# Optimization experiments

Hardware: AMD Instinct MI355X
Metric: run time of the kernel (lower is better)

Reference implementation:

```python
import jax, jax.numpy as jnp
import numpy as np

B, T, C, H = 4, 2048, 1024, 16
D = C // H  # head dim = 64

def setup_inputs() -> dict:
    key = jax.random.key(0)
    k1, k2, k3 = jax.random.split(key, 3)
    y = jax.random.normal(k1, (B, T, C), dtype=jnp.float32)
    W_attn = jax.random.normal(k2, (C, 3 * C), dtype=jnp.float32) * (1.0 / np.sqrt(C))
    b_attn = jnp.zeros((3 * C,), dtype=jnp.float32)
    W_proj = jax.random.normal(k3, (C, C), dtype=jnp.float32) * (1.0 / np.sqrt(C))
    b_proj = jnp.zeros((C,), dtype=jnp.float32)
    return {"y": y, "W_attn": W_attn, "b_attn": b_attn, "W_proj": W_proj, "b_proj": b_proj}

def reference(y, W_attn, b_attn, W_proj, b_proj):
    # qkv projection: [B,T,C] @ [C,3C] -> split into q,k,v
    qkv = y @ W_attn + b_attn
    q, k, v = jnp.split(qkv, 3, axis=-1)
    # [B,T,C] -> [B,H,T,D]
    q = q.reshape(B, T, H, D).swapaxes(1, 2)
    k = k.reshape(B, T, H, D).swapaxes(1, 2)
    v = v.reshape(B, T, H, D).swapaxes(1, 2)
    # scaled dot-product attention, non-causal (config default), dropout=0
    att = jnp.einsum('bhtd,bhrd->bhtr', q, k) * (1.0 / jnp.sqrt(jnp.float32(D)))
    att = jax.nn.softmax(att, axis=-1)
    out = jnp.einsum('bhts,bhsd->bhtd', att, v)
    out = out.swapaxes(1, 2).reshape(B, T, C)
    return out @ W_proj + b_proj
```

## Files before the change

kernel.cpp:

```cpp
#include <hip/hip_runtime.h>
#include <hip/hip_bf16.h>
#include <stdint.h>

#define B_ 4
#define T_ 2048
#define C_ 1024
#define H_ 16
#define D_ 64

typedef short bf16x8 __attribute__((ext_vector_type(8)));
typedef float f32x4 __attribute__((ext_vector_type(4)));
typedef unsigned short u16;

#define QSCALE 0.18033688011112042f

__device__ __forceinline__ u16 f2bf(float f) {
    __hip_bfloat16 h = __float2bfloat16(f);
    return *reinterpret_cast<u16*>(&h);
}

__device__ __forceinline__ float fexp2(float x) {
    float r;
    asm("v_exp_f32 %0, %1" : "=v"(r) : "v"(x));
    return r;
}

__device__ __forceinline__ void gload16(const void* g, void* l) {
    __builtin_amdgcn_global_load_lds(
        (const __attribute__((address_space(1))) unsigned int*)g,
        (__attribute__((address_space(3))) unsigned int*)l, 16, 0, 0);
}

__global__ void k_prep(const float* __restrict__ y, u16* __restrict__ y_bf,
                       const float* __restrict__ Wa, u16* __restrict__ WaT,
                       const float* __restrict__ Wp, u16* __restrict__ WpT) {
    const int bid = blockIdx.x, tid = threadIdx.x;
    if (bid < 8192) {
        int i = (bid * 256 + tid) * 4;
        float4 f = *reinterpret_cast<const float4*>(y + i);
        ushort4 o;
        o.x = f2bf(f.x); o.y = f2bf(f.y); o.z = f2bf(f.z); o.w = f2bf(f.w);
        *reinterpret_cast<ushort4*>(y_bf + i) = o;
        return;
    }
    __shared__ float tile[32][33];
    const float* src; u16* dst; int R, Cc, bx, by;
    if (bid < 8192 + 3072) {
        int idx = bid - 8192;
        src = Wa; dst = WaT; R = 1024; Cc = 3072;
        bx = idx % 96; by = idx / 96;
    } else {
        int idx = bid - 11264;
        src = Wp; dst = WpT; R = 1024; Cc = 1024;
        bx = idx & 31; by = idx >> 5;
    }
    int c0 = bx * 32, r0 = by * 32;
    int tx = tid & 31, ty = tid >> 5;
#pragma unroll
    for (int i = 0; i < 4; i++)
        tile[ty + i * 8][tx] = src[(size_t)(r0 + ty + i * 8) * Cc + c0 + tx];
    __syncthreads();
#pragma unroll
    for (int i = 0; i < 4; i++)
        dst[(size_t)(c0 + ty + i * 8) * R + r0 + tx] = f2bf(tile[tx][ty + i * 8]);
}

template <int EPI>
__launch_bounds__(256, 2)
__global__ void k_gemm(const u16* __restrict__ A, const u16* __restrict__ Bt,
                       const float* __restrict__ bias, int K, int N,
                       float* __restrict__ outf,
                       u16* __restrict__ qw, u16* __restrict__ kw, u16* __restrict__ vw) {
    __shared__ u16 As[128 * 64];
    __shared__ u16 Bs[128 * 64];
    const int tid = threadIdx.x;
    const int lane = tid & 63, w = tid >> 6;
    const int m0 = blockIdx.x * 128, n0 = blockIdx.y * 128;
    const int wm = (w >> 1) * 64, wn = (w & 1) * 64;
    const int lr = lane & 15, lg = lane >> 4;

    f32x4 acc[4][4];
#pragma unroll
    for (int i = 0; i < 4; i++)
#pragma unroll
        for (int j = 0; j < 4; j++) acc[i][j] = (f32x4){0.f, 0.f, 0.f, 0.f};

    const int nk = K >> 6;
    for (int kt = 0; kt < nk; ++kt) {
        const int k0 = kt * 64;
#pragma unroll
        for (int i = 0; i < 4; i++) {
            int c = i * 256 + tid;
            int row = c >> 3, k8 = (c & 7) << 3;
            gload16(A + (size_t)(m0 + row) * K + k0 + k8, (char*)As + i * 4096 + w * 1024);
            gload16(Bt + (size_t)(n0 + row) * K + k0 + k8, (char*)Bs + i * 4096 + w * 1024);
        }
        __syncthreads();
#pragma unroll
        for (int kk = 0; kk < 2; ++kk) {
            bf16x8 af[4], bfr[4];
#pragma unroll
            for (int mf = 0; mf < 4; ++mf)
                af[mf] = *reinterpret_cast<const bf16x8*>(&As[(wm + mf * 16 + lr) * 64 + kk * 32 + lg * 8]);
#pragma unroll
            for (int nf = 0; nf < 4; ++nf)
                bfr[nf] = *reinterpret_cast<const bf16x8*>(&Bs[(wn + nf * 16 + lr) * 64 + kk * 32 + lg * 8]);
#pragma unroll
            for (int mf = 0; mf < 4; ++mf)
#pragma unroll
                for (int nf = 0; nf < 4; ++nf)
                    acc[mf][nf] = __builtin_amdgcn_mfma_f32_16x16x32_bf16(af[mf], bfr[nf], acc[mf][nf], 0, 0, 0);
        }
        __syncthreads();
    }

    if (EPI == 0) {
#pragma unroll
        for (int mf = 0; mf < 4; ++mf)
#pragma unroll
            for (int nf = 0; nf < 4; ++nf) {
                int ng = n0 + wn + nf * 16 + lr;
                float bs = bias[ng];
#pragma unroll
                for (int r = 0; r < 4; ++r) {
                    int mg = m0 + wm + mf * 16 + lg * 4 + r;
                    outf[(size_t)mg * N + ng] = acc[mf][nf][r] + bs;
                }
            }
    } else {
        const int sec = n0 >> 10;
        const float sc = (sec == 0) ? QSCALE : 1.0f;
#pragma unroll
        for (int mf = 0; mf < 4; ++mf)
#pragma unroll
            for (int nf = 0; nf < 4; ++nf) {
                int ng = n0 + wn + nf * 16 + lr;
                float bs = bias[ng];
                int hd = ng & 1023;
                int h = hd >> 6, d = hd & 63;
                int mgb = m0 + wm + mf * 16 + lg * 4;
                int b = mgb >> 11, t0v = mgb & 2047;
                if (sec == 2) {
                    ushort4 pk;
                    pk.x = f2bf(acc[mf][nf][0] + bs);
                    pk.y = f2bf(acc[mf][nf][1] + bs);
                    pk.z = f2bf(acc[mf][nf][2] + bs);
                    pk.w = f2bf(acc[mf][nf][3] + bs);
                    *reinterpret_cast<ushort4*>(&vw[((size_t)(b * H_ + h) * D_ + d) * T_ + t0v]) = pk;
                } else {
                    u16* dst = (sec == 0) ? qw : kw;
#pragma unroll
                    for (int r = 0; r < 4; ++r)
                        dst[((size_t)(b * H_ + h) * T_ + t0v + r) * D_ + d] = f2bf((acc[mf][nf][r] + bs) * sc);
                }
            }
    }
}

__launch_bounds__(256, 4)
__global__ void k_attn(const u16* __restrict__ qw, const u16* __restrict__ kw,
                       const u16* __restrict__ vw, u16* __restrict__ attn) {
    __shared__ u16 Ks[2][64][64];
    __shared__ u16 Vs[2][64][64];
    const int tid = threadIdx.x, lane = tid & 63, w = tid >> 6;
    const int lr = lane & 15, lg = lane >> 4;
    const int bid = blockIdx.x;
    const int logical = (bid & 7) * 128 + (bid >> 3);
    const int bh = logical >> 4, qb = logical & 15;
    const int b = bh >> 4, h = bh & 15;
    const int q0 = qb * 128 + w * 32;
    const u16* qbase = qw + (size_t)bh * T_ * D_;
    const u16* kbase = kw + (size_t)bh * T_ * D_;
    const u16* vbase = vw + (size_t)bh * D_ * T_;

    bf16x8 qf[2][2];
#pragma unroll
    for (int jq = 0; jq < 2; jq++)
#pragma unroll
        for (int kd = 0; kd < 2; kd++)
            qf[jq][kd] = *reinterpret_cast<const bf16x8*>(
                &qbase[(size_t)(q0 + jq * 16 + lr) * D_ + kd * 32 + lg * 8]);

    auto stageK = [&](int kt, int buf) {
#pragma unroll
        for (int i = 0; i < 2; i++) {
            int idx = i * 256 + tid;
            int row = idx >> 3, ch = idx & 7;
            int gch = ch ^ ((row & 3) | (((row >> 3) & 1) << 2));
            gload16(kbase + ((size_t)(kt * 64 + row) * 64 + gch * 8),
                    (char*)&Ks[buf][0][0] + i * 4096 + w * 1024);
        }
    };
    auto stageV = [&](int kt, int buf) {
#pragma unroll
        for (int i = 0; i < 2; i++) {
            int idx = i * 256 + tid;
            int row = idx >> 3, ch = idx & 7;
            int gch = ch ^ (row & 7);
            gload16(vbase + ((size_t)row * T_ + kt * 64 + gch * 8),
                    (char*)&Vs[buf][0][0] + i * 4096 + w * 1024);
        }
    };

    f32x4 o[4][2];
#pragma unroll
    for (int md = 0; md < 4; md++)
#pragma unroll
        for (int jq = 0; jq < 2; jq++) o[md][jq] = (f32x4){0.f, 0.f, 0.f, 0.f};
    float l_run[2] = {0.f, 0.f};

    const int karow_base = ((lr >> 2) << 3) + (lr & 3);
    const int skl = ((lr & 3) | (((lr >> 2) & 1) << 2)) << 4;

    const int NT = T_ / 64;
    stageK(0, 0);
    stageV(0, 0);

    for (int kt = 0; kt < NT; ++kt) {
        const int cur = kt & 1;
        if (kt + 1 < NT) {
            stageK(kt + 1, cur ^ 1);
            stageV(kt + 1, cur ^ 1);
            asm volatile("s_waitcnt vmcnt(4)" ::: "memory");
        } else {
            asm volatile("s_waitcnt vmcnt(0)" ::: "memory");
        }
        __builtin_amdgcn_s_barrier();

        bf16x8 pfrag[2][2];
#pragma unroll
        for (int g = 0; g < 2; g++) {
            f32x4 st[2][2];
#pragma unroll
            for (int t = 0; t < 2; t++)
#pragma unroll
                for (int jq = 0; jq < 2; jq++) st[t][jq] = (f32x4){0.f, 0.f, 0.f, 0.f};
            __builtin_amdgcn_s_setprio(1);
#pragma unroll
            for (int t = 0; t < 2; t++) {
                int row = g * 32 + karow_base + t * 4;
#pragma unroll
                for (int kd = 0; kd < 2; kd++) {
                    bf16x8 ka = *reinterpret_cast<const bf16x8*>(
                        (const char*)&Ks[cur][0][0] + row * 128 + ((kd * 64 + lg * 16) ^ skl));
#pragma unroll
                    for (int jq = 0; jq < 2; jq++)
                        st[t][jq] = __builtin_amdgcn_mfma_f32_16x16x32_bf16(ka, qf[jq][kd], st[t][jq], 0, 0, 0);
                }
            }
            __builtin_amdgcn_s_setprio(0);
#pragma unroll
            for (int jq = 0; jq < 2; jq++) {
                float p0 = fexp2(st[0][jq][0]), p1 = fexp2(st[0][jq][1]);
                float p2 = fexp2(st[0][jq][2]), p3 = fexp2(st[0][jq][3]);
                float p4 = fexp2(st[1][jq][0]), p5 = fexp2(st[1][jq][1]);
                float p6 = fexp2(st[1][jq][2]), p7 = fexp2(st[1][jq][3]);
                l_run[jq] += ((p0 + p1) + (p2 + p3)) + ((p4 + p5) + (p6 + p7));
                pfrag[jq][g] = (bf16x8){(short)f2bf(p0), (short)f2bf(p1),
                                        (short)f2bf(p2), (short)f2bf(p3),
                                        (short)f2bf(p4), (short)f2bf(p5),
                                        (short)f2bf(p6), (short)f2bf(p7)};
            }
        }

#pragma unroll
        for (int g = 0; g < 2; g++) {
            bf16x8 va[4];
#pragma unroll
            for (int md = 0; md < 4; md++) {
                int row = md * 16 + lr;
                va[md] = *reinterpret_cast<const bf16x8*>(
                    (const char*)&Vs[cur][0][0] + row * 128 + ((g * 64 + lg * 16) ^ ((row & 7) << 4)));
            }
            __builtin_amdgcn_s_setprio(1);
#pragma unroll
            for (int md = 0; md < 4; md++)
#pragma unroll
                for (int jq = 0; jq < 2; jq++)
                    o[md][jq] = __builtin_amdgcn_mfma_f32_16x16x32_bf16(va[md], pfrag[jq][g], o[md][jq], 0, 0, 0);
            __builtin_amdgcn_s_setprio(0);
        }

        __builtin_amdgcn_s_barrier();
    }

#pragma unroll
    for (int jq = 0; jq < 2; jq++) {
        float l = l_run[jq];
        l += __shfl_xor(l, 16);
        l += __shfl_xor(l, 32);
        float rinv = 1.f / l;
        int q = q0 + jq * 16 + lr;
#pragma unroll
        for (int md = 0; md < 4; md++) {
            int d0 = md * 16 + lg * 4;
            ushort4 pk;
            pk.x = f2bf(o[md][jq][0] * rinv);
            pk.y = f2bf(o[md][jq][1] * rinv);
            pk.z = f2bf(o[md][jq][2] * rinv);
            pk.w = f2bf(o[md][jq][3] * rinv);
            *reinterpret_cast<ushort4*>(&attn[((size_t)(b * T_ + q)) * C_ + h * D_ + d0]) = pk;
        }
    }
}

extern "C" void kernel_launch(void* const* d_in, const int* in_sizes, int n_in,
                              void* d_out, int out_size, void* d_ws, size_t ws_size,
                              hipStream_t stream) {
    const float* y = (const float*)d_in[0];
    const float* W_attn = (const float*)d_in[1];
    const float* b_attn = (const float*)d_in[2];
    const float* W_proj = (const float*)d_in[3];
    const float* b_proj = (const float*)d_in[4];

    char* ws = (char*)d_ws;
    u16* y_bf = (u16*)(ws);
    u16* WaT  = (u16*)(ws + 16777216);
    u16* WpT  = (u16*)(ws + 16777216 + 6291456);
    u16* q_ws = (u16*)(ws + 25165824);
    u16* k_ws = (u16*)(ws + 25165824 + 16777216);
    u16* v_ws = (u16*)(ws + 25165824 + 33554432);
    u16* attn = (u16*)(ws + 25165824 + 50331648);

    k_prep<<<12288, 256, 0, stream>>>(y, y_bf, W_attn, WaT, W_proj, WpT);
    k_gemm<1><<<dim3(64, 24), 256, 0, stream>>>(y_bf, WaT, b_attn, 1024, 3072,
                                                nullptr, q_ws, k_ws, v_ws);
    k_attn<<<1024, 256, 0, stream>>>(q_ws, k_ws, v_ws, attn);
    k_gemm<0><<<dim3(64, 8), 256, 0, stream>>>(attn, WpT, b_proj, 1024, 1024,
                                               (float*)d_out, nullptr, nullptr, nullptr);
}
```

Measured before the change: 195.8 us.

## Software-pipeline attention loop: overlap PV of previous tile with QK/exp of current

Restructures the attention inner loop so the P·V MFMAs for tile k-1 are issued in the same phase as the QK^T MFMAs and exp for tile k. Two P-fragment register sets alternate, and the loop is unrolled by two. V gets a third LDS buffer so the previous V tile stays live while the next one is being loaded. The aim is to hide exp/convert latency behind matrix ops and give the scheduler more independent MFMA work, at the cost of extra registers and LDS that could reduce occupancy.

```diff
diff --git a/kernel.cpp b/kernel.cpp
--- a/kernel.cpp
+++ b/kernel.cpp
@@ -157,11 +157,75 @@
     }
 }
 
+#define ATTN_STAGE_K(kt, buf) do {                                            \
+    _Pragma("unroll") for (int i_ = 0; i_ < 2; i_++) {                        \
+        int idx_ = i_ * 256 + tid;                                            \
+        int row_ = idx_ >> 3, ch_ = idx_ & 7;                                 \
+        int gch_ = ch_ ^ ((row_ & 3) | (((row_ >> 3) & 1) << 2));             \
+        gload16(kbase + ((size_t)((kt) * 64 + row_) * 64 + gch_ * 8),         \
+                (char*)&Ks[0][0][0] + (buf) * 8192 + i_ * 4096 + w * 1024);   \
+    } } while (0)
+
+#define ATTN_STAGE_V(kt, buf) do {                                            \
+    _Pragma("unroll") for (int i_ = 0; i_ < 2; i_++) {                        \
+        int idx_ = i_ * 256 + tid;                                            \
+        int row_ = idx_ >> 3, ch_ = idx_ & 7;                                 \
+        int gch_ = ch_ ^ (row_ & 7);                                          \
+        gload16(vbase + ((size_t)row_ * T_ + (kt) * 64 + gch_ * 8),           \
+                (char*)&Vs[0][0][0] + (buf) * 8192 + i_ * 4096 + w * 1024);   \
+    } } while (0)
+
+#define ATTN_PV(PF) do {                                                      \
+    const char* Vp_ = (const char*)&Vs[0][0][0] + vprv * 8192;                \
+    __builtin_amdgcn_s_setprio(1);                                            \
+    _Pragma("unroll") for (int g_ = 0; g_ < 2; g_++) {                        \
+        _Pragma("unroll") for (int md_ = 0; md_ < 4; md_++) {                 \
+            int row_ = md_ * 16 + lr;                                         \
+            bf16x8 va_ = *reinterpret_cast<const bf16x8*>(                    \
+                Vp_ + row_ * 128 + ((g_ * 64 + lg * 16) ^ ((row_ & 7) << 4)));\
+            _Pragma("unroll") for (int jq_ = 0; jq_ < 2; jq_++)               \
+                o[md_][jq_] = __builtin_amdgcn_mfma_f32_16x16x32_bf16(        \
+                    va_, PF[jq_][g_], o[md_][jq_], 0, 0, 0);                  \
+        } }                                                                   \
+    __builtin_amdgcn_s_setprio(0); } while (0)
+
+#define ATTN_QKEXP(PF) do {                                                   \
+    const char* Kc_ = (const char*)&Ks[0][0][0] + kcur * 8192;                \
+    _Pragma("unroll") for (int g_ = 0; g_ < 2; g_++) {                        \
+        f32x4 st_[2][2];                                                      \
+        _Pragma("unroll") for (int t_ = 0; t_ < 2; t_++)                      \
+            _Pragma("unroll") for (int jq_ = 0; jq_ < 2; jq_++)               \
+                st_[t_][jq_] = (f32x4){0.f, 0.f, 0.f, 0.f};                   \
+        __builtin_amdgcn_s_setprio(1);                                        \
+        _Pragma("unroll") for (int t_ = 0; t_ < 2; t_++) {                    \
+            int row_ = g_ * 32 + karow_base + t_ * 4;                         \
+            _Pragma("unroll") for (int kd_ = 0; kd_ < 2; kd_++) {             \
+                bf16x8 ka_ = *reinterpret_cast<const bf16x8*>(                \
+                    Kc_ + row_ * 128 + ((kd_ * 64 + lg * 16) ^ skl));         \
+                _Pragma("unroll") for (int jq_ = 0; jq_ < 2; jq_++)           \
+                    st_[t_][jq_] = __builtin_amdgcn_mfma_f32_16x16x32_bf16(   \
+                        ka_, qf[jq_][kd_], st_[t_][jq_], 0, 0, 0);            \
+            } }                                                               \
+        __builtin_amdgcn_s_setprio(0);                                        \
+        _Pragma("unroll") for (int jq_ = 0; jq_ < 2; jq_++) {                 \
+            float p0_ = fexp2(st_[0][jq_][0]), p1_ = fexp2(st_[0][jq_][1]);   \
+            float p2_ = fexp2(st_[0][jq_][2]), p3_ = fexp2(st_[0][jq_][3]);   \
+            float p4_ = fexp2(st_[1][jq_][0]), p5_ = fexp2(st_[1][jq_][1]);   \
+            float p6_ = fexp2(st_[1][jq_][2]), p7_ = fexp2(st_[1][jq_][3]);   \
+            l_run[jq_] += ((p0_ + p1_) + (p2_ + p3_)) + ((p4_ + p5_) + (p6_ + p7_)); \
+            PF[jq_][g_] = (bf16x8){(short)f2bf(p0_), (short)f2bf(p1_),        \
+                                   (short)f2bf(p2_), (short)f2bf(p3_),        \
+                                   (short)f2bf(p4_), (short)f2bf(p5_),        \
+                                   (short)f2bf(p6_), (short)f2bf(p7_)};       \
+        } } } while (0)
+
+#define ATTN_VROT() do { vprv = vcur; vcur = vnxt; vnxt = (vnxt == 2) ? 0 : vnxt + 1; kcur ^= 1; } while (0)
+
 __launch_bounds__(256, 4)
 __global__ void k_attn(const u16* __restrict__ qw, const u16* __restrict__ kw,
                        const u16* __restrict__ vw, u16* __restrict__ attn) {
     __shared__ u16 Ks[2][64][64];
-    __shared__ u16 Vs[2][64][64];
+    __shared__ u16 Vs[3][64][64];
     const int tid = threadIdx.x, lane = tid & 63, w = tid >> 6;
     const int lr = lane & 15, lg = lane >> 4;
     const int bid = blockIdx.x;
@@ -181,107 +245,69 @@
             qf[jq][kd] = *reinterpret_cast<const bf16x8*>(
                 &qbase[(size_t)(q0 + jq * 16 + lr) * D_ + kd * 32 + lg * 8]);
 
-    auto stageK = [&](int kt, int buf) {
-#pragma unroll
-        for (int i = 0; i < 2; i++) {
-            int idx = i * 256 + tid;
-            int row = idx >> 3, ch = idx & 7;
-            int gch = ch ^ ((row & 3) | (((row >> 3) & 1) << 2));
-            gload16(kbase + ((size_t)(kt * 64 + row) * 64 + gch * 8),
-                    (char*)&Ks[buf][0][0] + i * 4096 + w * 1024);
-        }
-    };
-    auto stageV = [&](int kt, int buf) {
-#pragma unroll
-        for (int i = 0; i < 2; i++) {
-            int idx = i * 256 + tid;
-            int row = idx >> 3, ch = idx & 7;
-            int gch = ch ^ (row & 7);
-            gload16(vbase + ((size_t)row * T_ + kt * 64 + gch * 8),
-                    (char*)&Vs[buf][0][0] + i * 4096 + w * 1024);
-        }
-    };
-
     f32x4 o[4][2];
 #pragma unroll
     for (int md = 0; md < 4; md++)
 #pragma unroll
         for (int jq = 0; jq < 2; jq++) o[md][jq] = (f32x4){0.f, 0.f, 0.f, 0.f};
     float l_run[2] = {0.f, 0.f};
+    bf16x8 pfA[2][2], pfB[2][2];
 
     const int karow_base = ((lr >> 2) << 3) + (lr & 3);
     const int skl = ((lr & 3) | (((lr >> 2) & 1) << 2)) << 4;
 
-    const int NT = T_ / 64;
-    stageK(0, 0);
-    stageV(0, 0);
-
-    for (int kt = 0; kt < NT; ++kt) {
-        const int cur = kt & 1;
-        if (kt + 1 < NT) {
-            stageK(kt + 1, cur ^ 1);
-            stageV(kt + 1, cur ^ 1);
-            asm volatile("s_waitcnt vmcnt(4)" ::: "memory");
-        } else {
-            asm volatile("s_waitcnt vmcnt(0)" ::: "memory");
-        }
+    int kcur = 0, vprv = 2, vcur = 0, vnxt = 1;
+
+    ATTN_STAGE_K(0, 0);
+    ATTN_STAGE_V(0, 0);
+
+    ATTN_STAGE_K(1, 1);
+    ATTN_STAGE_V(1, 1);
+    asm volatile("s_waitcnt vmcnt(6)" ::: "memory");
+    __builtin_amdgcn_s_barrier();
+    ATTN_QKEXP(pfA);
+    __builtin_amdgcn_s_barrier();
+    ATTN_VROT();
+
+    for (int it = 0; it < 15; ++it) {
+        ATTN_STAGE_K(2 * it + 2, kcur ^ 1);
+        ATTN_STAGE_V(2 * it + 2, vnxt);
+        asm volatile("s_waitcnt vmcnt(6)" ::: "memory");
         __builtin_amdgcn_s_barrier();
-
-        bf16x8 pfrag[2][2];
-#pragma unroll
-        for (int g = 0; g < 2; g++) {
-            f32x4 st[2][2];
-#pragma unroll
-            for (int t = 0; t < 2; t++)
-#pragma unroll
-                for (int jq = 0; jq < 2; jq++) st[t][jq] = (f32x4){0.f, 0.f, 0.f, 0.f};
-            __builtin_amdgcn_s_setprio(1);
-#pragma unroll
-            for (int t = 0; t < 2; t++) {
-                int row = g * 32 + karow_base + t * 4;
-#pragma unroll
-                for (int kd = 0; kd < 2; kd++) {
-                    bf16x8 ka = *reinterpret_cast<const bf16x8*>(
-                        (const char*)&Ks[cur][0][0] + row * 128 + ((kd * 64 + lg * 16) ^ skl));
-#pragma unroll
-                    for (int jq = 0; jq < 2; jq++)
-                        st[t][jq] = __builtin_amdgcn_mfma_f32_16x16x32_bf16(ka, qf[jq][kd], st[t][jq], 0, 0, 0);
-                }
-            }
-            __builtin_amdgcn_s_setprio(0);
-#pragma unroll
-            for (int jq = 0; jq < 2; jq++) {
-                float p0 = fexp2(st[0][jq][0]), p1 = fexp2(st[0][jq][1]);
-                float p2 = fexp2(st[0][jq][2]), p3 = fexp2(st[0][jq][3]);
-                float p4 = fexp2(st[1][jq][0]), p5 = fexp2(st[1][jq][1]);
-                float p6 = fexp2(st[1][jq][2]), p7 = fexp2(st[1][jq][3]);
-                l_run[jq] += ((p0 + p1) + (p2 + p3)) + ((p4 + p5) + (p6 + p7));
-                pfrag[jq][g] = (bf16x8){(short)f2bf(p0), (short)f2bf(p1),
-                                        (short)f2bf(p2), (short)f2bf(p3),
-                                        (short)f2bf(p4), (short)f2bf(p5),
-                                        (short)f2bf(p6), (short)f2bf(p7)};
-            }
-        }
-
-#pragma unroll
-        for (int g = 0; g < 2; g++) {
-            bf16x8 va[4];
+        ATTN_PV(pfA);
+        ATTN_QKEXP(pfB);
+        __builtin_amdgcn_s_barrier();
+        ATTN_VROT();
+
+        ATTN_STAGE_K(2 * it + 3, kcur ^ 1);
+        ATTN_STAGE_V(2 * it + 3, vnxt);
+        asm volatile("s_waitcnt vmcnt(6)" ::: "memory");
+        __builtin_amdgcn_s_barrier();
+        ATTN_PV(pfB);
+        ATTN_QKEXP(pfA);
+        __builtin_amdgcn_s_barrier();
+        ATTN_VROT();
+    }
+
+    asm volatile("s_waitcnt vmcnt(0)" ::: "memory");
+    __builtin_amdgcn_s_barrier();
+    ATTN_PV(pfA);
+    ATTN_QKEXP(pfB);
+    {
+        const char* Vf = (const char*)&Vs[0][0][0] + vcur * 8192;
+        __builtin_amdgcn_s_setprio(1);
+#pragma unroll
+        for (int g = 0; g < 2; g++)
 #pragma unroll
             for (int md = 0; md < 4; md++) {
                 int row = md * 16 + lr;
-                va[md] = *reinterpret_cast<const bf16x8*>(
-                    (const char*)&Vs[cur][0][0] + row * 128 + ((g * 64 + lg * 16) ^ ((row & 7) << 4)));
+                bf16x8 va = *reinterpret_cast<const bf16x8*>(
+                    Vf + row * 128 + ((g * 64 + lg * 16) ^ ((row & 7) << 4)));
+#pragma unroll
+                for (int jq = 0; jq < 2; jq++)
+                    o[md][jq] = __builtin_amdgcn_mfma_f32_16x16x32_bf16(va, pfB[jq][g], o[md][jq], 0, 0, 0);
             }
-            __builtin_amdgcn_s_setprio(1);
-#pragma unroll
-            for (int md = 0; md < 4; md++)
-#pragma unroll
-                for (int jq = 0; jq < 2; jq++)
-                    o[md][jq] = __builtin_amdgcn_mfma_f32_16x16x32_bf16(va[md], pfrag[jq][g], o[md][jq], 0, 0, 0);
-            __builtin_amdgcn_s_setprio(0);
-        }
-
-        __builtin_amdgcn_s_barrier();
+        __builtin_amdgcn_s_setprio(0);
     }
 
 #pragma unroll
```

Result: no change. 192.7 us (-1.6%).
